# Kernel optimization log

Hardware: AMD Instinct MI355X
Metric: run time of the kernel (lower is better)

## Reference

```python
import jax, jax.numpy as jnp
import numpy as np

NUM_HEAD = 12
DIM_MODEL = 768
HEAD_DIM = DIM_MODEL // NUM_HEAD


def setup_inputs() -> dict:
    key = jax.random.key(0)
    ks = jax.random.split(key, 4)
    B, S, D = 2, 2048, DIM_MODEL
    scale = 1.0 / np.sqrt(D)
    return {
        "v1": jax.random.normal(ks[0], (B, S, D), dtype=jnp.float32),
        "v1_mask": jnp.zeros((B, 1, 1, S), dtype=jnp.float32),
        "Wq": jax.random.normal(ks[1], (D, D), dtype=jnp.float32) * scale,
        "bq": jnp.zeros((D,), dtype=jnp.float32),
        "Wk": jax.random.normal(ks[2], (D, D), dtype=jnp.float32) * scale,
        "bk": jnp.zeros((D,), dtype=jnp.float32),
        "Wv": jax.random.normal(ks[3], (D, D), dtype=jnp.float32) * scale,
        "bv": jnp.zeros((D,), dtype=jnp.float32),
    }


def reference(v1, v1_mask, Wq, bq, Wk, bk, Wv, bv):
    B, S, D = v1.shape
    H, hd = NUM_HEAD, HEAD_DIM

    def split_heads(x):  # [B,S,D] -> [B,H,S,hd]
        return x.reshape(B, S, H, hd).transpose(0, 2, 1, 3)

    q = split_heads(v1 @ Wq + bq)
    k = split_heads(v1 @ Wk + bk)
    v = split_heads(v1 @ Wv + bv)

    scores = jnp.einsum("bhqd,bhkd->bhqk", q, k) / jnp.sqrt(jnp.float32(hd))
    scores = scores + v1_mask  # additive mask broadcasts over heads/query
    probs = jax.nn.softmax(scores, axis=-1)
    # dropout is identity in eval/reference mode
    ctx = jnp.einsum("bhqk,bhkd->bhqd", probs, v)
    return ctx.transpose(0, 2, 1, 3).reshape(B, S, D)
```

## Files before the change

### kernel.cpp

```cpp
#include <hip/hip_runtime.h>
#include <math.h>

#define B_SZ 2
#define S_SZ 2048
#define D_SZ 768
#define NH   12
#define HD   64
#define BH_T (B_SZ * NH)
#define M_TOT (B_SZ * S_SZ)

using bfrag = __attribute__((ext_vector_type(8))) short;
using ffrag = __attribute__((ext_vector_type(4))) float;

__device__ __forceinline__ unsigned short f2bf(float f) {
    unsigned int u = __float_as_uint(f);
    u += 0x7fffu + ((u >> 16) & 1u);
    return (unsigned short)(u >> 16);
}
__device__ __forceinline__ unsigned short f2bf_fast(float f) {
    return (unsigned short)((__float_as_uint(f) + 0x8000u) >> 16);
}

__device__ __forceinline__ void async16(void* lds, const void* gp) {
    __builtin_amdgcn_global_load_lds(
        (const __attribute__((address_space(1))) unsigned int*)gp,
        (__attribute__((address_space(3))) unsigned int*)lds,
        16, 0, 0);
}

__global__ __launch_bounds__(256) void prep(
    const float* __restrict__ v1,
    const float* __restrict__ Wq, const float* __restrict__ Wk,
    const float* __restrict__ Wv,
    unsigned short* __restrict__ v1b, unsigned short* __restrict__ Wt) {
    __shared__ float tile[64][65];
    const int bx = blockIdx.x;
    const int t = threadIdx.x;
    if (bx < 3072) {
        int i = (bx * 256 + t) * 4;
        float4 v = *(const float4*)&v1[i];
        ushort4 o;
        o.x = f2bf(v.x); o.y = f2bf(v.y); o.z = f2bf(v.z); o.w = f2bf(v.w);
        *(ushort4*)&v1b[i] = o;
    } else {
        int r = bx - 3072;
        int z = r / 144;
        int rr = r % 144;
        int n0 = (rr % 12) * 64, k0 = (rr / 12) * 64;
        const float* W = (z == 0) ? Wq : (z == 1) ? Wk : Wv;
        unsigned short* dst = Wt + (size_t)z * D_SZ * D_SZ;
        #pragma unroll
        for (int i = 0; i < 16; ++i) {
            int flat = i * 256 + t;
            int rr2 = flat >> 6, c = flat & 63;
            tile[rr2][c] = W[(size_t)(k0 + rr2) * D_SZ + n0 + c];
        }
        __syncthreads();
        #pragma unroll
        for (int i = 0; i < 16; ++i) {
            int flat = i * 256 + t;
            int rr2 = flat >> 6, c = flat & 63;
            dst[(size_t)(n0 + rr2) * D_SZ + k0 + c] = f2bf(tile[c][rr2]);
        }
    }
}

#define CP_LD 136
#define CPV_LD 72

__global__ __launch_bounds__(256) void proj_gemm(
    const unsigned short* __restrict__ Ab,
    const unsigned short* __restrict__ Wt,
    const float* __restrict__ bq, const float* __restrict__ bk_,
    const float* __restrict__ bv_,
    unsigned short* __restrict__ Qb, unsigned short* __restrict__ Kb,
    unsigned short* __restrict__ Vtb) {
    const int z = blockIdx.z;
    const unsigned short* Bt = Wt + (size_t)z * D_SZ * D_SZ;
    const float* bias = (z == 0) ? bq : (z == 1) ? bk_ : bv_;

    __shared__ unsigned short smem[2][64 * 64 + 128 * 64];
    const int t = threadIdx.x;
    const int lane = t & 63;
    const int w = t >> 6;
    const int wm = w & 1, wn = w >> 1;
    const int col = lane & 15;
    const int quad = lane >> 4;
    const int m0 = blockIdx.y * 64;
    const int n0 = blockIdx.x * 128;
    const int wbase = t & ~63;

    ffrag acc[2][4];
    #pragma unroll
    for (int i = 0; i < 2; ++i)
        #pragma unroll
        for (int j = 0; j < 4; ++j) { ffrag zf = {0.f, 0.f, 0.f, 0.f}; acc[i][j] = zf; }

    #pragma unroll
    for (int i = 0; i < 2; ++i) {
        int c = i * 256 + t;
        int row = c >> 3;
        int gcol = ((c & 7) ^ (row & 7)) * 8;
        async16(&smem[0][(size_t)(i * 256 + wbase) * 8],
                &Ab[(size_t)(m0 + row) * D_SZ + gcol]);
    }
    #pragma unroll
    for (int i = 0; i < 4; ++i) {
        int c = i * 256 + t;
        int row = c >> 3;
        int gcol = ((c & 7) ^ (row & 7)) * 8;
        async16(&smem[0][64 * 64 + (size_t)(i * 256 + wbase) * 8],
                &Bt[(size_t)(n0 + row) * D_SZ + gcol]);
    }

    const int nIter = D_SZ / 64;
    for (int it = 0; it < nIter; ++it) {
        const int cur = it & 1;
        __syncthreads();
        if (it + 1 < nIter) {
            const int kn = (it + 1) * 64;
            #pragma unroll
            for (int i = 0; i < 2; ++i) {
                int c = i * 256 + t;
                int row = c >> 3;
                int gcol = ((c & 7) ^ (row & 7)) * 8;
                async16(&smem[cur ^ 1][(size_t)(i * 256 + wbase) * 8],
                        &Ab[(size_t)(m0 + row) * D_SZ + kn + gcol]);
            }
            #pragma unroll
            for (int i = 0; i < 4; ++i) {
                int c = i * 256 + t;
                int row = c >> 3;
                int gcol = ((c & 7) ^ (row & 7)) * 8;
                async16(&smem[cur ^ 1][64 * 64 + (size_t)(i * 256 + wbase) * 8],
                        &Bt[(size_t)(n0 + row) * D_SZ + kn + gcol]);
            }
        }
        const unsigned short* As = &smem[cur][0];
        const unsigned short* Bs = &smem[cur][64 * 64];
        #pragma unroll
        for (int kk = 0; kk < 64; kk += 32) {
            const int cc = (kk >> 3) + quad;
            bfrag a[2], b[4];
            #pragma unroll
            for (int mi = 0; mi < 2; ++mi) {
                int row = wm * 32 + mi * 16 + col;
                a[mi] = *(const bfrag*)&As[row * 64 + ((cc ^ (row & 7)) * 8)];
            }
            #pragma unroll
            for (int ni = 0; ni < 4; ++ni) {
                int row = wn * 64 + ni * 16 + col;
                b[ni] = *(const bfrag*)&Bs[row * 64 + ((cc ^ (row & 7)) * 8)];
            }
            if (z == 2) {
                #pragma unroll
                for (int mi = 0; mi < 2; ++mi)
                    #pragma unroll
                    for (int ni = 0; ni < 4; ++ni)
                        acc[mi][ni] = __builtin_amdgcn_mfma_f32_16x16x32_bf16(
                            a[mi], b[ni], acc[mi][ni], 0, 0, 0);
            } else {
                #pragma unroll
                for (int mi = 0; mi < 2; ++mi)
                    #pragma unroll
                    for (int ni = 0; ni < 4; ++ni)
                        acc[mi][ni] = __builtin_amdgcn_mfma_f32_16x16x32_bf16(
                            b[ni], a[mi], acc[mi][ni], 0, 0, 0);
            }
        }
    }

    __syncthreads();
    unsigned short* rp = &smem[0][0];

    if (z < 2) {
        const float sc = (z == 0) ? 0.125f : 1.0f;
        #pragma unroll
        for (int mi = 0; mi < 2; ++mi) {
            int m_local = wm * 32 + mi * 16 + col;
            #pragma unroll
            for (int ni = 0; ni < 4; ++ni) {
                int n_base = wn * 64 + ni * 16 + quad * 4;
                float4 b4 = *(const float4*)&bias[n0 + n_base];
                uint2 pk;
                pk.x = (unsigned)f2bf((acc[mi][ni][0] + b4.x) * sc) |
                       ((unsigned)f2bf((acc[mi][ni][1] + b4.y) * sc) << 16);
                pk.y = (unsigned)f2bf((acc[mi][ni][2] + b4.z) * sc) |
                       ((unsigned)f2bf((acc[mi][ni][3] + b4.w) * sc) << 16);
                *(uint2*)&rp[m_local * CP_LD + n_base] = pk;
            }
        }
        __syncthreads();
        unsigned short* Out = (z == 0) ? Qb : Kb;
        #pragma unroll
        for (int j = 0; j < 4; ++j) {
            int flat = j * 256 + t;
            int row = flat >> 4;
            int ch = flat & 15;
            uint4 vv = *(const uint4*)&rp[row * CP_LD + ch * 8];
            int m = m0 + row;
            int bb = m >> 11, s = m & 2047;
            int h = (n0 >> 6) + (ch >> 3);
            int d = (ch & 7) * 8;
            *(uint4*)&Out[((size_t)(bb * NH + h) * S_SZ + s) * HD + d] = vv;
        }
    } else {
        #pragma unroll
        for (int ni = 0; ni < 4; ++ni) {
            int n_local = wn * 64 + ni * 16 + col;
            float bvv = bias[n0 + n_local];
            #pragma unroll
            for (int mi = 0; mi < 2; ++mi) {
                int m_base = wm * 32 + mi * 16 + quad * 4;
                uint2 pk;
                pk.x = (unsigned)f2bf(acc[mi][ni][0] + bvv) |
                       ((unsigned)f2bf(acc[mi][ni][1] + bvv) << 16);
                pk.y = (unsigned)f2bf(acc[mi][ni][2] + bvv) |
                       ((unsigned)f2bf(acc[mi][ni][3] + bvv) << 16);
                *(uint2*)&rp[n_local * CPV_LD + m_base] = pk;
            }
        }
        __syncthreads();
        #pragma unroll
        for (int j = 0; j < 4; ++j) {
            int flat = j * 256 + t;
            int row = flat >> 3;
            int ch = flat & 7;
            uint4 vv = *(const uint4*)&rp[row * CPV_LD + ch * 8];
            int n = n0 + row;
            int h = n >> 6, d = n & 63;
            int m = m0 + ch * 8;
            int bb = m >> 11, s = m & 2047;
            *(uint4*)&Vtb[((size_t)(bb * NH + h) * HD + d) * S_SZ + s] = vv;
        }
    }
}

__global__ __launch_bounds__(256) void attn_mfma(
    const unsigned short* __restrict__ Qb, const unsigned short* __restrict__ Kb,
    const unsigned short* __restrict__ Vt, const float* __restrict__ mask,
    float* __restrict__ out) {
    __shared__ unsigned short Ks[2][64 * 64];
    __shared__ unsigned short Vs[2][64 * 64];
    __shared__ unsigned short Ps[4][16 * 64];

    const int t = threadIdx.x;
    const int lane = t & 63;
    const int w = t >> 6;
    const int col = lane & 15;
    const int quad = lane >> 4;
    const int q0 = blockIdx.x * 64;
    const int bh = blockIdx.y;
    const int b = bh / NH, h = bh % NH;
    const int wbase = t & ~63;

    const unsigned short* Qg = Qb + (size_t)bh * S_SZ * HD;
    const unsigned short* Kg = Kb + (size_t)bh * S_SZ * HD;
    const unsigned short* Vg = Vt + (size_t)bh * S_SZ * HD;
    const float* mrow = mask + (size_t)b * S_SZ;

    const int arow = w * 16 + col;
    bfrag aq[2];
    #pragma unroll
    for (int kk = 0; kk < 2; ++kk)
        aq[kk] = *(const bfrag*)&Qg[(size_t)(q0 + arow) * HD + (kk * 4 + quad) * 8];

    int srw[2], sgc[2];
    #pragma unroll
    for (int i = 0; i < 2; ++i) {
        int c = i * 256 + t;
        srw[i] = c >> 3;
        sgc[i] = ((c & 7) ^ (srw[i] & 7)) * 8;
    }

    #pragma unroll
    for (int i = 0; i < 2; ++i) {
        async16(&Ks[0][(size_t)(i * 256 + wbase) * 8],
                &Kg[(size_t)srw[i] * HD + sgc[i]]);
        async16(&Vs[0][(size_t)(i * 256 + wbase) * 8],
                &Vg[(size_t)srw[i] * S_SZ + sgc[i]]);
    }
    float mcur[4], mnext[4];
    #pragma unroll
    for (int ni = 0; ni < 4; ++ni) mcur[ni] = mrow[ni * 16 + col];

    ffrag o[4];
    #pragma unroll
    for (int i = 0; i < 4; ++i) { ffrag zf = {0.f, 0.f, 0.f, 0.f}; o[i] = zf; }
    float lsum[4] = {0.f, 0.f, 0.f, 0.f};

    const int nIter = S_SZ / 64;
    for (int it = 0; it < nIter; ++it) {
        const int cur = it & 1;
        __syncthreads();
        if (it + 1 < nIter) {
            const int kn = (it + 1) * 64;
            #pragma unroll
            for (int i = 0; i < 2; ++i) {
                async16(&Ks[cur ^ 1][(size_t)(i * 256 + wbase) * 8],
                        &Kg[(size_t)(kn + srw[i]) * HD + sgc[i]]);
                async16(&Vs[cur ^ 1][(size_t)(i * 256 + wbase) * 8],
                        &Vg[(size_t)srw[i] * S_SZ + kn + sgc[i]]);
            }
            #pragma unroll
            for (int ni = 0; ni < 4; ++ni) mnext[ni] = mrow[kn + ni * 16 + col];
        }

        ffrag s[4];
        #pragma unroll
        for (int i = 0; i < 4; ++i) { ffrag zf = {0.f, 0.f, 0.f, 0.f}; s[i] = zf; }
        #pragma unroll
        for (int kk = 0; kk < 2; ++kk) {
            const int cc = kk * 4 + quad;
            #pragma unroll
            for (int ni = 0; ni < 4; ++ni) {
                int brow = ni * 16 + col;
                bfrag bk8 = *(const bfrag*)&Ks[cur][brow * 64 + ((cc ^ (brow & 7)) * 8)];
                s[ni] = __builtin_amdgcn_mfma_f32_16x16x32_bf16(aq[kk], bk8, s[ni], 0, 0, 0);
            }
        }

        #pragma unroll
        for (int ni = 0; ni < 4; ++ni) {
            #pragma unroll
            for (int r = 0; r < 4; ++r) {
                float e = __expf(s[ni][r] + mcur[ni]);
                s[ni][r] = e;
                lsum[r] += e;
            }
        }

        unsigned short* Pw = &Ps[w][0];
        #pragma unroll
        for (int ni = 0; ni < 4; ++ni) {
            #pragma unroll
            for (int r = 0; r < 4; ++r) {
                int prow = quad * 4 + r;
                int pcol = ni * 16 + col;
                Pw[prow * 64 + (((pcol >> 3) ^ (prow & 7)) * 8) + (pcol & 7)] =
                    f2bf_fast(s[ni][r]);
            }
        }
        #pragma unroll
        for (int kk = 0; kk < 2; ++kk) {
            const int cc = kk * 4 + quad;
            bfrag ap = *(const bfrag*)&Pw[col * 64 + ((cc ^ (col & 7)) * 8)];
            #pragma unroll
            for (int di = 0; di < 4; ++di) {
                int vrow = di * 16 + col;
                bfrag bv8 = *(const bfrag*)&Vs[cur][vrow * 64 + ((cc ^ (vrow & 7)) * 8)];
                o[di] = __builtin_amdgcn_mfma_f32_16x16x32_bf16(ap, bv8, o[di], 0, 0, 0);
            }
        }

        #pragma unroll
        for (int ni = 0; ni < 4; ++ni) mcur[ni] = mnext[ni];
    }

    #pragma unroll
    for (int r = 0; r < 4; ++r) {
        #pragma unroll
        for (int off = 1; off < 16; off <<= 1)
            lsum[r] += __shfl_xor(lsum[r], off);
    }
    float inv[4];
    #pragma unroll
    for (int r = 0; r < 4; ++r) inv[r] = 1.0f / lsum[r];
    #pragma unroll
    for (int di = 0; di < 4; ++di) {
        int d = di * 16 + col;
        #pragma unroll
        for (int r = 0; r < 4; ++r) {
            int q = q0 + w * 16 + quad * 4 + r;
            out[((size_t)(b * S_SZ + q)) * D_SZ + h * HD + d] = o[di][r] * inv[r];
        }
    }
}

extern "C" void kernel_launch(void* const* d_in, const int* in_sizes, int n_in,
                              void* d_out, int out_size, void* d_ws, size_t ws_size,
                              hipStream_t stream) {
    const float* v1   = (const float*)d_in[0];
    const float* mask = (const float*)d_in[1];
    const float* Wq   = (const float*)d_in[2];
    const float* bq   = (const float*)d_in[3];
    const float* Wk   = (const float*)d_in[4];
    const float* bk   = (const float*)d_in[5];
    const float* Wv   = (const float*)d_in[6];
    const float* bv   = (const float*)d_in[7];
    float* out = (float*)d_out;

    char* ws = (char*)d_ws;
    const size_t per_b = (size_t)BH_T * S_SZ * HD * 2;
    unsigned short* Qb  = (unsigned short*)(ws);
    unsigned short* Kb  = (unsigned short*)(ws + per_b);
    unsigned short* Vtb = (unsigned short*)(ws + 2 * per_b);
    unsigned short* v1b = (unsigned short*)(ws + 3 * per_b);
    unsigned short* Wt  = (unsigned short*)(ws + 3 * per_b + (size_t)M_TOT * D_SZ * 2);

    prep<<<dim3(3072 + 432), 256, 0, stream>>>(v1, Wq, Wk, Wv, v1b, Wt);
    proj_gemm<<<dim3(6, 64, 3), 256, 0, stream>>>(v1b, Wt, bq, bk, bv, Qb, Kb, Vtb);
    attn_mfma<<<dim3(32, 24), 256, 0, stream>>>(Qb, Kb, Vtb, mask, out);
}
```

Before: 160.1 us.

## Shrink projection GEMM tile, drop double buffering, transpose QK^T MFMA in attention

The projection GEMM now uses 32-row M tiles with a single LDS buffer and synchronous load-then-compute, which doubles the grid and lowers LDS use per block to raise occupancy. In the attention kernel, the QK^T MFMA swaps its operands so each lane holds scores for one query row across four keys. This lets the mask load as float4, the P tile be stored as packed uint2 writes, and the row sum be reduced with fewer shuffles. The cost is losing load/compute overlap in the GEMM and reading each weight tile more times across the larger grid.

```diff
diff --git a/kernel.cpp b/kernel.cpp
--- a/kernel.cpp
+++ b/kernel.cpp
@@ -66,7 +66,7 @@
 }
 
 #define CP_LD 136
-#define CPV_LD 72
+#define CPV_LD 40
 
 __global__ __launch_bounds__(256) void proj_gemm(
     const unsigned short* __restrict__ Ab,
@@ -79,73 +79,45 @@
     const unsigned short* Bt = Wt + (size_t)z * D_SZ * D_SZ;
     const float* bias = (z == 0) ? bq : (z == 1) ? bk_ : bv_;
 
-    __shared__ unsigned short smem[2][64 * 64 + 128 * 64];
+    __shared__ unsigned short smem[32 * 64 + 128 * 64];
+    unsigned short* As = smem;
+    unsigned short* Bs = smem + 32 * 64;
+
     const int t = threadIdx.x;
     const int lane = t & 63;
     const int w = t >> 6;
     const int wm = w & 1, wn = w >> 1;
     const int col = lane & 15;
     const int quad = lane >> 4;
-    const int m0 = blockIdx.y * 64;
+    const int m0 = blockIdx.y * 32;
     const int n0 = blockIdx.x * 128;
     const int wbase = t & ~63;
 
-    ffrag acc[2][4];
-    #pragma unroll
-    for (int i = 0; i < 2; ++i)
-        #pragma unroll
-        for (int j = 0; j < 4; ++j) { ffrag zf = {0.f, 0.f, 0.f, 0.f}; acc[i][j] = zf; }
-
-    #pragma unroll
-    for (int i = 0; i < 2; ++i) {
-        int c = i * 256 + t;
-        int row = c >> 3;
-        int gcol = ((c & 7) ^ (row & 7)) * 8;
-        async16(&smem[0][(size_t)(i * 256 + wbase) * 8],
-                &Ab[(size_t)(m0 + row) * D_SZ + gcol]);
-    }
-    #pragma unroll
-    for (int i = 0; i < 4; ++i) {
-        int c = i * 256 + t;
-        int row = c >> 3;
-        int gcol = ((c & 7) ^ (row & 7)) * 8;
-        async16(&smem[0][64 * 64 + (size_t)(i * 256 + wbase) * 8],
-                &Bt[(size_t)(n0 + row) * D_SZ + gcol]);
-    }
-
-    const int nIter = D_SZ / 64;
-    for (int it = 0; it < nIter; ++it) {
-        const int cur = it & 1;
-        __syncthreads();
-        if (it + 1 < nIter) {
-            const int kn = (it + 1) * 64;
-            #pragma unroll
-            for (int i = 0; i < 2; ++i) {
-                int c = i * 256 + t;
-                int row = c >> 3;
-                int gcol = ((c & 7) ^ (row & 7)) * 8;
-                async16(&smem[cur ^ 1][(size_t)(i * 256 + wbase) * 8],
-                        &Ab[(size_t)(m0 + row) * D_SZ + kn + gcol]);
-            }
-            #pragma unroll
-            for (int i = 0; i < 4; ++i) {
-                int c = i * 256 + t;
-                int row = c >> 3;
-                int gcol = ((c & 7) ^ (row & 7)) * 8;
-                async16(&smem[cur ^ 1][64 * 64 + (size_t)(i * 256 + wbase) * 8],
-                        &Bt[(size_t)(n0 + row) * D_SZ + kn + gcol]);
-            }
-        }
-        const unsigned short* As = &smem[cur][0];
-        const unsigned short* Bs = &smem[cur][64 * 64];
+    ffrag acc[4];
+    #pragma unroll
+    for (int j = 0; j < 4; ++j) { ffrag zf = {0.f, 0.f, 0.f, 0.f}; acc[j] = zf; }
+
+    const int arow = t >> 3, agc = ((t & 7) ^ (arow & 7)) * 8;
+
+    for (int k0 = 0; k0 < D_SZ; k0 += 64) {
+        __syncthreads();
+        async16(&As[(size_t)wbase * 8], &Ab[(size_t)(m0 + arow) * D_SZ + k0 + agc]);
+        #pragma unroll
+        for (int i = 0; i < 4; ++i) {
+            int c = i * 256 + t;
+            int row = c >> 3;
+            int gcol = ((c & 7) ^ (row & 7)) * 8;
+            async16(&Bs[(size_t)(i * 256 + wbase) * 8],
+                    &Bt[(size_t)(n0 + row) * D_SZ + k0 + gcol]);
+        }
+        __syncthreads();
         #pragma unroll
         for (int kk = 0; kk < 64; kk += 32) {
             const int cc = (kk >> 3) + quad;
-            bfrag a[2], b[4];
-            #pragma unroll
-            for (int mi = 0; mi < 2; ++mi) {
-                int row = wm * 32 + mi * 16 + col;
-                a[mi] = *(const bfrag*)&As[row * 64 + ((cc ^ (row & 7)) * 8)];
+            bfrag a, b[4];
+            {
+                int row = wm * 16 + col;
+                a = *(const bfrag*)&As[row * 64 + ((cc ^ (row & 7)) * 8)];
             }
             #pragma unroll
             for (int ni = 0; ni < 4; ++ni) {
@@ -154,50 +126,42 @@
             }
             if (z == 2) {
                 #pragma unroll
-                for (int mi = 0; mi < 2; ++mi)
-                    #pragma unroll
-                    for (int ni = 0; ni < 4; ++ni)
-                        acc[mi][ni] = __builtin_amdgcn_mfma_f32_16x16x32_bf16(
-                            a[mi], b[ni], acc[mi][ni], 0, 0, 0);
+                for (int ni = 0; ni < 4; ++ni)
+                    acc[ni] = __builtin_amdgcn_mfma_f32_16x16x32_bf16(
+                        a, b[ni], acc[ni], 0, 0, 0);
             } else {
                 #pragma unroll
-                for (int mi = 0; mi < 2; ++mi)
-                    #pragma unroll
-                    for (int ni = 0; ni < 4; ++ni)
-                        acc[mi][ni] = __builtin_amdgcn_mfma_f32_16x16x32_bf16(
-                            b[ni], a[mi], acc[mi][ni], 0, 0, 0);
+                for (int ni = 0; ni < 4; ++ni)
+                    acc[ni] = __builtin_amdgcn_mfma_f32_16x16x32_bf16(
+                        b[ni], a, acc[ni], 0, 0, 0);
             }
         }
     }
 
     __syncthreads();
-    unsigned short* rp = &smem[0][0];
 
     if (z < 2) {
         const float sc = (z == 0) ? 0.125f : 1.0f;
-        #pragma unroll
-        for (int mi = 0; mi < 2; ++mi) {
-            int m_local = wm * 32 + mi * 16 + col;
-            #pragma unroll
-            for (int ni = 0; ni < 4; ++ni) {
-                int n_base = wn * 64 + ni * 16 + quad * 4;
-                float4 b4 = *(const float4*)&bias[n0 + n_base];
-                uint2 pk;
-                pk.x = (unsigned)f2bf((acc[mi][ni][0] + b4.x) * sc) |
-                       ((unsigned)f2bf((acc[mi][ni][1] + b4.y) * sc) << 16);
-                pk.y = (unsigned)f2bf((acc[mi][ni][2] + b4.z) * sc) |
-                       ((unsigned)f2bf((acc[mi][ni][3] + b4.w) * sc) << 16);
-                *(uint2*)&rp[m_local * CP_LD + n_base] = pk;
-            }
+        const int m_local = wm * 16 + col;
+        #pragma unroll
+        for (int ni = 0; ni < 4; ++ni) {
+            int n_base = wn * 64 + ni * 16 + quad * 4;
+            float4 b4 = *(const float4*)&bias[n0 + n_base];
+            uint2 pk;
+            pk.x = (unsigned)f2bf((acc[ni][0] + b4.x) * sc) |
+                   ((unsigned)f2bf((acc[ni][1] + b4.y) * sc) << 16);
+            pk.y = (unsigned)f2bf((acc[ni][2] + b4.z) * sc) |
+                   ((unsigned)f2bf((acc[ni][3] + b4.w) * sc) << 16);
+            *(uint2*)&smem[m_local * CP_LD + n_base] = pk;
         }
         __syncthreads();
         unsigned short* Out = (z == 0) ? Qb : Kb;
         #pragma unroll
-        for (int j = 0; j < 4; ++j) {
+        for (int j = 0; j < 2; ++j) {
             int flat = j * 256 + t;
             int row = flat >> 4;
             int ch = flat & 15;
-            uint4 vv = *(const uint4*)&rp[row * CP_LD + ch * 8];
+            uint4 vv = *(const uint4*)&smem[row * CP_LD + ch * 8];
             int m = m0 + row;
             int bb = m >> 11, s = m & 2047;
             int h = (n0 >> 6) + (ch >> 3);
@@ -209,24 +173,20 @@
         for (int ni = 0; ni < 4; ++ni) {
             int n_local = wn * 64 + ni * 16 + col;
             float bvv = bias[n0 + n_local];
-            #pragma unroll
-            for (int mi = 0; mi < 2; ++mi) {
-                int m_base = wm * 32 + mi * 16 + quad * 4;
-                uint2 pk;
-                pk.x = (unsigned)f2bf(acc[mi][ni][0] + bvv) |
-                       ((unsigned)f2bf(acc[mi][ni][1] + bvv) << 16);
-                pk.y = (unsigned)f2bf(acc[mi][ni][2] + bvv) |
-                       ((unsigned)f2bf(acc[mi][ni][3] + bvv) << 16);
-                *(uint2*)&rp[n_local * CPV_LD + m_base] = pk;
-            }
-        }
-        __syncthreads();
-        #pragma unroll
-        for (int j = 0; j < 4; ++j) {
+            uint2 pk;
+            pk.x = (unsigned)f2bf(acc[ni][0] + bvv) |
+                   ((unsigned)f2bf(acc[ni][1] + bvv) << 16);
+            pk.y = (unsigned)f2bf(acc[ni][2] + bvv) |
+                   ((unsigned)f2bf(acc[ni][3] + bvv) << 16);
+            *(uint2*)&smem[n_local * CPV_LD + wm * 16 + quad * 4] = pk;
+        }
+        __syncthreads();
+        #pragma unroll
+        for (int j = 0; j < 2; ++j) {
             int flat = j * 256 + t;
-            int row = flat >> 3;
-            int ch = flat & 7;
-            uint4 vv = *(const uint4*)&rp[row * CPV_LD + ch * 8];
+            int row = flat >> 2;
+            int ch = flat & 3;
+            uint4 vv = *(const uint4*)&smem[row * CPV_LD + ch * 8];
             int n = n0 + row;
             int h = n >> 6, d = n & 63;
             int m = m0 + ch * 8;
@@ -280,14 +240,15 @@
         async16(&Vs[0][(size_t)(i * 256 + wbase) * 8],
                 &Vg[(size_t)srw[i] * S_SZ + sgc[i]]);
     }
-    float mcur[4], mnext[4];
-    #pragma unroll
-    for (int ni = 0; ni < 4; ++ni) mcur[ni] = mrow[ni * 16 + col];
+    float4 mcur[4], mnext[4];
+    #pragma unroll
+    for (int ni = 0; ni < 4; ++ni)
+        mcur[ni] = *(const float4*)&mrow[ni * 16 + quad * 4];
 
     ffrag o[4];
     #pragma unroll
     for (int i = 0; i < 4; ++i) { ffrag zf = {0.f, 0.f, 0.f, 0.f}; o[i] = zf; }
-    float lsum[4] = {0.f, 0.f, 0.f, 0.f};
+    float lsum = 0.f;
 
     const int nIter = S_SZ / 64;
     for (int it = 0; it < nIter; ++it) {
@@ -303,7 +264,8 @@
                         &Vg[(size_t)srw[i] * S_SZ + kn + sgc[i]]);
             }
             #pragma unroll
-            for (int ni = 0; ni < 4; ++ni) mnext[ni] = mrow[kn + ni * 16 + col];
+            for (int ni = 0; ni < 4; ++ni)
+                mnext[ni] = *(const float4*)&mrow[kn + ni * 16 + quad * 4];
         }
 
         ffrag s[4];
@@ -315,8 +277,8 @@
             #pragma unroll
             for (int ni = 0; ni < 4; ++ni) {
                 int brow = ni * 16 + col;
-                bfrag bk8 = *(const bfrag*)&Ks[cur][brow * 64 + ((cc ^ (brow & 7)) * 8)];
-                s[ni] = __builtin_amdgcn_mfma_f32_16x16x32_bf16(aq[kk], bk8, s[ni], 0, 0, 0);
+                bfrag kf = *(const bfrag*)&Ks[cur][brow * 64 + ((cc ^ (brow & 7)) * 8)];
+                s[ni] = __builtin_amdgcn_mfma_f32_16x16x32_bf16(kf, aq[kk], s[ni], 0, 0, 0);
             }
         }
 
@@ -324,23 +286,24 @@
         for (int ni = 0; ni < 4; ++ni) {
             #pragma unroll
             for (int r = 0; r < 4; ++r) {
-                float e = __expf(s[ni][r] + mcur[ni]);
+                float e = __expf(s[ni][r] + ((const float*)&mcur[ni])[r]);
                 s[ni][r] = e;
-                lsum[r] += e;
+                lsum += e;
             }
         }
 
         unsigned short* Pw = &Ps[w][0];
         #pragma unroll
         for (int ni = 0; ni < 4; ++ni) {
-            #pragma unroll
-            for (int r = 0; r < 4; ++r) {
-                int prow = quad * 4 + r;
-                int pcol = ni * 16 + col;
-                Pw[prow * 64 + (((pcol >> 3) ^ (prow & 7)) * 8) + (pcol & 7)] =
-                    f2bf_fast(s[ni][r]);
-            }
-        }
+            uint2 pk;
+            pk.x = (unsigned)f2bf_fast(s[ni][0]) |
+                   ((unsigned)f2bf_fast(s[ni][1]) << 16);
+            pk.y = (unsigned)f2bf_fast(s[ni][2]) |
+                   ((unsigned)f2bf_fast(s[ni][3]) << 16);
+            int phys = (((ni * 2 + (quad >> 1)) ^ (col & 7)) * 8) + ((quad & 1) * 4);
+            *(uint2*)&Pw[col * 64 + phys] = pk;
+        }
+
         #pragma unroll
         for (int kk = 0; kk < 2; ++kk) {
             const int cc = kk * 4 + quad;
@@ -357,15 +320,11 @@
         for (int ni = 0; ni < 4; ++ni) mcur[ni] = mnext[ni];
     }
 
-    #pragma unroll
-    for (int r = 0; r < 4; ++r) {
-        #pragma unroll
-        for (int off = 1; off < 16; off <<= 1)
-            lsum[r] += __shfl_xor(lsum[r], off);
-    }
+    lsum += __shfl_xor(lsum, 16);
+    lsum += __shfl_xor(lsum, 32);
     float inv[4];
     #pragma unroll
-    for (int r = 0; r < 4; ++r) inv[r] = 1.0f / lsum[r];
+    for (int r = 0; r < 4; ++r) inv[r] = 1.0f / __shfl(lsum, quad * 4 + r);
     #pragma unroll
     for (int di = 0; di < 4; ++di) {
         int d = di * 16 + col;
@@ -399,6 +358,6 @@
     unsigned short* Wt  = (unsigned short*)(ws + 3 * per_b + (size_t)M_TOT * D_SZ * 2);
 
     prep<<<dim3(3072 + 432), 256, 0, stream>>>(v1, Wq, Wk, Wv, v1b, Wt);
-    proj_gemm<<<dim3(6, 64, 3), 256, 0, stream>>>(v1b, Wt, bq, bk, bv, Qb, Kb, Vtb);
+    proj_gemm<<<dim3(6, 128, 3), 256, 0, stream>>>(v1b, Wt, bq, bk, bv, Qb, Kb, Vtb);
     attn_mfma<<<dim3(32, 24), 256, 0, stream>>>(Qb, Kb, Vtb, mask, out);
 }
```

Measured after the change: 169.9 us. 1.06x slower.

## Split attention over key dimension with atomic accumulation and normalize pass

Applied to the files above, without the earlier changes.

Splits the key sequence into four chunks, each handled by its own block, which multiplies the grid fourfold to expose more parallelism. Blocks atomically add their unnormalized partial outputs into a zeroed output and write partial softmax row sums. A separate normalize kernel then divides by the combined sums. This drops the K/V double buffering and adds a memset, fp32 atomics on the full output and an extra pass over it, all of which raise memory traffic and synchronisation cost.

```diff
diff --git a/kernel.cpp b/kernel.cpp
--- a/kernel.cpp
+++ b/kernel.cpp
@@ -8,6 +8,8 @@
 #define HD   64
 #define BH_T (B_SZ * NH)
 #define M_TOT (B_SZ * S_SZ)
+#define NSPLIT 4
+#define LPS ((size_t)B_SZ * NH * S_SZ)
 
 using bfrag = __attribute__((ext_vector_type(8))) short;
 using ffrag = __attribute__((ext_vector_type(4))) float;
@@ -239,9 +241,9 @@
 __global__ __launch_bounds__(256) void attn_mfma(
     const unsigned short* __restrict__ Qb, const unsigned short* __restrict__ Kb,
     const unsigned short* __restrict__ Vt, const float* __restrict__ mask,
-    float* __restrict__ out) {
-    __shared__ unsigned short Ks[2][64 * 64];
-    __shared__ unsigned short Vs[2][64 * 64];
+    float* __restrict__ out, float* __restrict__ lp) {
+    __shared__ unsigned short Ks[64 * 64];
+    __shared__ unsigned short Vs[64 * 64];
     __shared__ unsigned short Ps[4][16 * 64];
 
     const int t = threadIdx.x;
@@ -251,6 +253,7 @@
     const int quad = lane >> 4;
     const int q0 = blockIdx.x * 64;
     const int bh = blockIdx.y;
+    const int split = blockIdx.z;
     const int b = bh / NH, h = bh % NH;
     const int wbase = t & ~63;
 
@@ -273,38 +276,26 @@
         sgc[i] = ((c & 7) ^ (srw[i] & 7)) * 8;
     }
 
-    #pragma unroll
-    for (int i = 0; i < 2; ++i) {
-        async16(&Ks[0][(size_t)(i * 256 + wbase) * 8],
-                &Kg[(size_t)srw[i] * HD + sgc[i]]);
-        async16(&Vs[0][(size_t)(i * 256 + wbase) * 8],
-                &Vg[(size_t)srw[i] * S_SZ + sgc[i]]);
-    }
-    float mcur[4], mnext[4];
-    #pragma unroll
-    for (int ni = 0; ni < 4; ++ni) mcur[ni] = mrow[ni * 16 + col];
-
     ffrag o[4];
     #pragma unroll
     for (int i = 0; i < 4; ++i) { ffrag zf = {0.f, 0.f, 0.f, 0.f}; o[i] = zf; }
     float lsum[4] = {0.f, 0.f, 0.f, 0.f};
 
-    const int nIter = S_SZ / 64;
-    for (int it = 0; it < nIter; ++it) {
-        const int cur = it & 1;
-        __syncthreads();
-        if (it + 1 < nIter) {
-            const int kn = (it + 1) * 64;
-            #pragma unroll
-            for (int i = 0; i < 2; ++i) {
-                async16(&Ks[cur ^ 1][(size_t)(i * 256 + wbase) * 8],
-                        &Kg[(size_t)(kn + srw[i]) * HD + sgc[i]]);
-                async16(&Vs[cur ^ 1][(size_t)(i * 256 + wbase) * 8],
-                        &Vg[(size_t)srw[i] * S_SZ + kn + sgc[i]]);
-            }
-            #pragma unroll
-            for (int ni = 0; ni < 4; ++ni) mnext[ni] = mrow[kn + ni * 16 + col];
-        }
+    const int kbeg = split * (S_SZ / NSPLIT);
+    for (int it = 0; it < S_SZ / NSPLIT / 64; ++it) {
+        const int k0 = kbeg + it * 64;
+        __syncthreads();
+        #pragma unroll
+        for (int i = 0; i < 2; ++i) {
+            async16(&Ks[(size_t)(i * 256 + wbase) * 8],
+                    &Kg[(size_t)(k0 + srw[i]) * HD + sgc[i]]);
+            async16(&Vs[(size_t)(i * 256 + wbase) * 8],
+                    &Vg[(size_t)srw[i] * S_SZ + k0 + sgc[i]]);
+        }
+        float mcur[4];
+        #pragma unroll
+        for (int ni = 0; ni < 4; ++ni) mcur[ni] = mrow[k0 + ni * 16 + col];
+        __syncthreads();
 
         ffrag s[4];
         #pragma unroll
@@ -315,7 +306,7 @@
             #pragma unroll
             for (int ni = 0; ni < 4; ++ni) {
                 int brow = ni * 16 + col;
-                bfrag bk8 = *(const bfrag*)&Ks[cur][brow * 64 + ((cc ^ (brow & 7)) * 8)];
+                bfrag bk8 = *(const bfrag*)&Ks[brow * 64 + ((cc ^ (brow & 7)) * 8)];
                 s[ni] = __builtin_amdgcn_mfma_f32_16x16x32_bf16(aq[kk], bk8, s[ni], 0, 0, 0);
             }
         }
@@ -348,13 +339,10 @@
             #pragma unroll
             for (int di = 0; di < 4; ++di) {
                 int vrow = di * 16 + col;
-                bfrag bv8 = *(const bfrag*)&Vs[cur][vrow * 64 + ((cc ^ (vrow & 7)) * 8)];
+                bfrag bv8 = *(const bfrag*)&Vs[vrow * 64 + ((cc ^ (vrow & 7)) * 8)];
                 o[di] = __builtin_amdgcn_mfma_f32_16x16x32_bf16(ap, bv8, o[di], 0, 0, 0);
             }
         }
-
-        #pragma unroll
-        for (int ni = 0; ni < 4; ++ni) mcur[ni] = mnext[ni];
     }
 
     #pragma unroll
@@ -363,18 +351,40 @@
         for (int off = 1; off < 16; off <<= 1)
             lsum[r] += __shfl_xor(lsum[r], off);
     }
-    float inv[4];
-    #pragma unroll
-    for (int r = 0; r < 4; ++r) inv[r] = 1.0f / lsum[r];
+
     #pragma unroll
     for (int di = 0; di < 4; ++di) {
         int d = di * 16 + col;
         #pragma unroll
         for (int r = 0; r < 4; ++r) {
             int q = q0 + w * 16 + quad * 4 + r;
-            out[((size_t)(b * S_SZ + q)) * D_SZ + h * HD + d] = o[di][r] * inv[r];
-        }
-    }
+            atomicAdd(&out[((size_t)(b * S_SZ + q)) * D_SZ + h * HD + d], o[di][r]);
+        }
+    }
+    if (col == 0) {
+        #pragma unroll
+        for (int r = 0; r < 4; ++r) {
+            int q = q0 + w * 16 + quad * 4 + r;
+            lp[(size_t)split * LPS + ((size_t)b * NH + h) * S_SZ + q] = lsum[r];
+        }
+    }
+}
+
+__global__ __launch_bounds__(256) void normalize(
+    float* __restrict__ out, const float* __restrict__ lp) {
+    int i4 = blockIdx.x * 256 + threadIdx.x;
+    int flat = i4 * 4;
+    int b = flat / (S_SZ * D_SZ);
+    int rem = flat % (S_SZ * D_SZ);
+    int q = rem / D_SZ;
+    int c = rem % D_SZ;
+    int h = c >> 6;
+    size_t base = ((size_t)b * NH + h) * S_SZ + q;
+    float l = lp[base] + lp[LPS + base] + lp[2 * LPS + base] + lp[3 * LPS + base];
+    float inv = 1.0f / l;
+    float4 v = *(const float4*)&out[flat];
+    v.x *= inv; v.y *= inv; v.z *= inv; v.w *= inv;
+    *(float4*)&out[flat] = v;
 }
 
 extern "C" void kernel_launch(void* const* d_in, const int* in_sizes, int n_in,
@@ -397,8 +407,11 @@
     unsigned short* Vtb = (unsigned short*)(ws + 2 * per_b);
     unsigned short* v1b = (unsigned short*)(ws + 3 * per_b);
     unsigned short* Wt  = (unsigned short*)(ws + 3 * per_b + (size_t)M_TOT * D_SZ * 2);
+    float* lp = (float*)(ws + 3 * per_b);
 
     prep<<<dim3(3072 + 432), 256, 0, stream>>>(v1, Wq, Wk, Wv, v1b, Wt);
     proj_gemm<<<dim3(6, 64, 3), 256, 0, stream>>>(v1b, Wt, bq, bk, bv, Qb, Kb, Vtb);
-    attn_mfma<<<dim3(32, 24), 256, 0, stream>>>(Qb, Kb, Vtb, mask, out);
-}
+    hipMemsetAsync(out, 0, (size_t)out_size * sizeof(float), stream);
+    attn_mfma<<<dim3(32, 24, NSPLIT), 256, 0, stream>>>(Qb, Kb, Vtb, mask, out, lp);
+    normalize<<<dim3((M_TOT * D_SZ) / 1024), 256, 0, stream>>>(out, lp);
+}
```

Result: slower. 170.7 us (+6.6%).
